# Performance work log

Hardware: AMD Instinct MI355X
Metric: run time of the kernel (lower is better)

## Reference

```python
import jax, jax.numpy as jnp
import numpy as np

C = 512
NUM_GROUPS = 32
EPS = 1e-6


def setup_inputs() -> dict:
    key = jax.random.key(0)
    ks = jax.random.split(key, 6)
    B, H, W = 4, 64, 64
    x = jax.random.normal(ks[0], (B, H, W, C), dtype=jnp.float32)
    # GroupNorm affine params (flax default init: scale=1, bias=0)
    gn_scale = jnp.ones((C,), jnp.float32)
    gn_bias = jnp.zeros((C,), jnp.float32)
    # 1x1 convs == per-pixel dense layers; weight [C_in, C_out], bias [C_out]
    def dense(k):
        return jax.random.normal(k, (C, C), dtype=jnp.float32) * 0.02
    wq, wk, wv, wo = dense(ks[1]), dense(ks[2]), dense(ks[3]), dense(ks[4])
    bq = jnp.zeros((C,), jnp.float32)
    bk = jnp.zeros((C,), jnp.float32)
    bv = jnp.zeros((C,), jnp.float32)
    bo = jnp.zeros((C,), jnp.float32)
    return {"x": x, "gn_scale": gn_scale, "gn_bias": gn_bias,
            "wq": wq, "bq": bq, "wk": wk, "bk": bk,
            "wv": wv, "bv": bv, "wo": wo, "bo": bo}


def _group_norm(x, scale, bias):
    B, H, W, Cc = x.shape
    g = NUM_GROUPS
    xg = x.reshape(B, H, W, g, Cc // g)
    mean = jnp.mean(xg, axis=(1, 2, 4), keepdims=True)
    var = jnp.var(xg, axis=(1, 2, 4), keepdims=True)
    xn = (xg - mean) * jax.lax.rsqrt(var + EPS)
    xn = xn.reshape(B, H, W, Cc)
    return xn * scale + bias


def reference(x, gn_scale, gn_bias, wq, bq, wk, bk, wv, bv, wo, bo):
    B, H, W, Cc = x.shape
    hn = _group_norm(x, gn_scale, gn_bias)
    # 1x1 convs
    q = (hn @ wq + bq).reshape(B, H * W, Cc)
    k = (hn @ wk + bk).reshape(B, H * W, Cc)
    v = (hn @ wv + bv).reshape(B, H * W, Cc)
    scale = jnp.asarray(Cc, x.dtype) ** -0.5
    # scores[b,i,j] = <q_i, k_j> * c^-0.5; softmax over keys j
    attn = jax.nn.softmax(jnp.einsum('bic,bjc->bij', q, k) * scale, axis=-1)
    out = jnp.einsum('bij,bjc->bic', attn, v).reshape(B, H, W, Cc)
    return x + (out @ wo + bo)
```

## Files before the change

kernel.cpp:

```cpp
#include <hip/hip_runtime.h>


typedef __attribute__((ext_vector_type(8))) __bf16 bf16x8;
typedef __attribute__((ext_vector_type(4))) __bf16 bf16x4;
typedef __attribute__((ext_vector_type(4))) float  floatx4;

#define C_DIM 512
#define SPB   4096
#define MTOT  16384

#define HN_OFF  ((size_t)0)
#define Q_OFF   ((size_t)16 << 20)
#define K_OFF   ((size_t)32 << 20)
#define V4_OFF  ((size_t)48 << 20)
#define WT_OFF  ((size_t)64 << 20)
#define O1_OFF  ((size_t)68 << 20)
#define ML_OFF  ((size_t)84 << 20)
#define GS_OFF  (ML_OFF + (size_t)(256 << 10))

__device__ inline floatx4 mfma16(bf16x8 a, bf16x8 b, floatx4 c) {
    return __builtin_amdgcn_mfma_f32_16x16x32_bf16(a, b, c, 0, 0, 0);
}

__device__ inline void gload16(const void* g, void* lds) {
    __builtin_amdgcn_global_load_lds(
        (const __attribute__((address_space(1))) unsigned int*)g,
        (__attribute__((address_space(3))) unsigned int*)lds, 16, 0, 0);
}

__global__ __launch_bounds__(256) void zero_stats(float* gstats) {
    gstats[threadIdx.x] = 0.f;
}

__global__ __launch_bounds__(256) void gn_stats(
    const float* __restrict__ x, float* __restrict__ gstats) {
    int bg = blockIdx.x;
    int b = bg >> 5, g = bg & 31;
    int tid = threadIdx.x;
    int cq = tid & 3, s0 = tid >> 2;
    const float* base = x + (size_t)b * SPB * C_DIM + g * 16 + cq * 4
                          + (size_t)blockIdx.y * 1024 * C_DIM;
    float sum = 0.f, sq = 0.f;
#pragma unroll 4
    for (int i = 0; i < 16; ++i) {
        floatx4 v = *(const floatx4*)(base + (size_t)(i * 64 + s0) * C_DIM);
        sum += v[0] + v[1] + v[2] + v[3];
        sq  += v[0]*v[0] + v[1]*v[1] + v[2]*v[2] + v[3]*v[3];
    }
#pragma unroll
    for (int off = 1; off < 64; off <<= 1) {
        sum += __shfl_xor(sum, off);
        sq  += __shfl_xor(sq,  off);
    }
    __shared__ float sm[8];
    int w = tid >> 6, lane = tid & 63;
    if (lane == 0) { sm[w] = sum; sm[4 + w] = sq; }
    __syncthreads();
    if (tid == 0) {
        atomicAdd(&gstats[bg * 2],     sm[0] + sm[1] + sm[2] + sm[3]);
        atomicAdd(&gstats[bg * 2 + 1], sm[4] + sm[5] + sm[6] + sm[7]);
    }
}

__global__ __launch_bounds__(256) void gn_apply(
    const float* __restrict__ x, const float* __restrict__ gstats,
    const float* __restrict__ gsc, const float* __restrict__ gbi,
    __bf16* __restrict__ hn) {
    int bg = blockIdx.x;
    int b = bg >> 5, g = bg & 31;
    int tid = threadIdx.x;
    int cq = tid & 3, s0 = tid >> 2;
    float S  = gstats[bg * 2], Qs = gstats[bg * 2 + 1];
    float mean = S * (1.f / 65536.f);
    float var  = Qs * (1.f / 65536.f) - mean * mean;
    float rstd = rsqrtf(var + 1e-6f);
    float sc[4], bi[4];
#pragma unroll
    for (int j = 0; j < 4; ++j) {
        float s_ = gsc[g * 16 + cq * 4 + j] * rstd;
        sc[j] = s_;
        bi[j] = gbi[g * 16 + cq * 4 + j] - mean * s_;
    }
    size_t off = (size_t)b * SPB * C_DIM + g * 16 + cq * 4
               + (size_t)blockIdx.y * 1024 * C_DIM;
    const float* base = x + off;
    __bf16* hbase = hn + off;
#pragma unroll 4
    for (int i = 0; i < 16; ++i) {
        floatx4 v = *(const floatx4*)(base + (size_t)(i * 64 + s0) * C_DIM);
        bf16x4 o;
#pragma unroll
        for (int j = 0; j < 4; ++j) o[j] = (__bf16)(v[j] * sc[j] + bi[j]);
        *(bf16x4*)(hbase + (size_t)(i * 64 + s0) * C_DIM) = o;
    }
}

__global__ __launch_bounds__(256) void wt_kernel(
    const float* __restrict__ w0, const float* __restrict__ w1,
    const float* __restrict__ w2, const float* __restrict__ w3,
    __bf16* __restrict__ wt) {
    const float* srcs[4] = {w0, w1, w2, w3};
    const float* src = srcs[blockIdx.z];
    __bf16* dst = wt + (size_t)blockIdx.z * C_DIM * C_DIM;
    __shared__ float tile[32][33];
    int tx = threadIdx.x & 31, ty = threadIdx.x >> 5;
    int gx = blockIdx.x * 32, gy = blockIdx.y * 32;
#pragma unroll
    for (int i = 0; i < 4; ++i)
        tile[ty + i * 8][tx] = src[(size_t)(gy + ty + i * 8) * C_DIM + gx + tx];
    __syncthreads();
#pragma unroll
    for (int i = 0; i < 4; ++i) {
        int n = gx + ty + i * 8;
        int k = gy + tx;
        dst[(size_t)n * C_DIM + k] = (__bf16)tile[tx][ty + i * 8];
    }
}

__global__ __launch_bounds__(256, 2) void proj_qkv(
    const __bf16* __restrict__ hn, const __bf16* __restrict__ wt_all,
    const float* __restrict__ bq, const float* __restrict__ bk,
    const float* __restrict__ bv, __bf16* __restrict__ qout,
    __bf16* __restrict__ kout, __bf16* __restrict__ v4out) {
    int z = blockIdx.z;
    const __bf16* wt = wt_all + (size_t)z * C_DIM * C_DIM;
    const float* bias = (z == 0) ? bq : (z == 1) ? bk : bv;
    __shared__ __bf16 Alds[128 * 32];
    __shared__ __bf16 Blds[128 * 32];
    int tid = threadIdx.x, lane = tid & 63, w = tid >> 6;
    int c = lane & 15, quad = lane >> 4;
    int wm = w & 1, wn = w >> 1;
    int mbase = blockIdx.x * 128, nbase = blockIdx.y * 128;
    floatx4 acc[4][4] = {};
    for (int kb = 0; kb < 16; ++kb) {
        __syncthreads();
#pragma unroll
        for (int p = 0; p < 2; ++p) {
            int chunk0 = w * 128 + p * 64;
            int chunk = chunk0 + lane;
            int row = chunk >> 2, qk = chunk & 3;
            gload16(hn + (size_t)(mbase + row) * C_DIM + kb * 32 + qk * 8, Alds + chunk0 * 8);
            gload16(wt + (size_t)(nbase + row) * C_DIM + kb * 32 + qk * 8, Blds + chunk0 * 8);
        }
        __syncthreads();
        bf16x8 af[4], bfr[4];
#pragma unroll
        for (int mt = 0; mt < 4; ++mt)
            af[mt] = *(const bf16x8*)(Alds + (wm * 64 + mt * 16 + c) * 32 + quad * 8);
#pragma unroll
        for (int nt = 0; nt < 4; ++nt)
            bfr[nt] = *(const bf16x8*)(Blds + (wn * 64 + nt * 16 + c) * 32 + quad * 8);
#pragma unroll
        for (int mt = 0; mt < 4; ++mt)
#pragma unroll
            for (int nt = 0; nt < 4; ++nt)
                acc[mt][nt] = mfma16(af[mt], bfr[nt], acc[mt][nt]);
    }
    float scale = (z == 0) ? 0.0441941738241592f : 1.0f;
#pragma unroll
    for (int nt = 0; nt < 4; ++nt) {
        int n = nbase + wn * 64 + nt * 16 + c;
        float bval = bias[n];
#pragma unroll
        for (int mt = 0; mt < 4; ++mt) {
            int m0 = mbase + wm * 64 + mt * 16 + quad * 4;
#pragma unroll
            for (int r = 0; r < 4; ++r) {
                int m = m0 + r;
                float val = (acc[mt][nt][r] + bval) * scale;
                if (z == 0)      qout[(size_t)m * C_DIM + n] = (__bf16)val;
                else if (z == 1) kout[(size_t)m * C_DIM + n] = (__bf16)val;
                else {
                    int bb = m >> 12, pos = m & 4095;
                    v4out[((size_t)(bb * 512 + (pos >> 3)) * C_DIM + n) * 8 + (pos & 7)] = (__bf16)val;
                }
            }
        }
    }
}

__device__ inline void stage_K(const __bf16* kbase, int key0,
                               __bf16* Klds, int w, int lane) {
#pragma unroll
    for (int p = 0; p < 8; ++p) {
        int chunk0 = w * 512 + p * 64;
        int chunk = chunk0 + lane;
        gload16(kbase + (size_t)(key0 + (chunk & 31)) * C_DIM + (chunk >> 5) * 8,
                Klds + chunk0 * 8);
    }
}

__device__ inline void stage_V(const __bf16* vsrc, __bf16* Vlds, int w, int lane) {
#pragma unroll
    for (int p = 0; p < 8; ++p) {
        int chunk0 = w * 512 + p * 64;
        gload16(vsrc + (size_t)(chunk0 + lane) * 8, Vlds + chunk0 * 8);
    }
}

__global__ __launch_bounds__(256, 2) void flash_kernel(
    const __bf16* __restrict__ q, const __bf16* __restrict__ kmat,
    const __bf16* __restrict__ v4, __bf16* __restrict__ op0,
    __bf16* __restrict__ op1, float* __restrict__ lpart) {
    __shared__ __bf16 Klds[16384];
    __shared__ __bf16 Vlds[16384];
    __shared__ __bf16 Plds[64 * 40];
    int tid = threadIdx.x, lane = tid & 63, w = tid >> 6;
    int c = lane & 15, quad = lane >> 4;
    int bid = blockIdx.x;
    int h = bid & 1, qt = (bid >> 1) & 63, b = bid >> 7;

    const __bf16* qp = q + ((size_t)(b * SPB + qt * 64 + w * 16 + c)) * C_DIM + quad * 8;
    bf16x8 qf[16];
#pragma unroll
    for (int ks = 0; ks < 16; ++ks) qf[ks] = *(const bf16x8*)(qp + ks * 32);
    floatx4 o[4][8];
#pragma unroll
    for (int mg = 0; mg < 4; ++mg)
#pragma unroll
        for (int t = 0; t < 8; ++t) o[mg][t] = (floatx4){0.f, 0.f, 0.f, 0.f};
    float l_r[4] = {0.f, 0.f, 0.f, 0.f};

    const __bf16* kbase = kmat + (size_t)b * SPB * C_DIM;
    const __bf16* vbase = v4 + (size_t)b * 512 * C_DIM * 8;

    stage_K(kbase, h * 2048, Klds, w, lane);
    __syncthreads();

    for (int kt = 0; kt < 64; ++kt) {
        int key0 = h * 2048 + kt * 32;
        stage_V(vbase + (size_t)(key0 >> 3) * C_DIM * 8, Vlds, w, lane);
        floatx4 s0 = (floatx4){0.f,0.f,0.f,0.f}, s1 = (floatx4){0.f,0.f,0.f,0.f};
#pragma unroll
        for (int ks = 0; ks < 16; ++ks) {
            bf16x8 k0 = *(const bf16x8*)(Klds + (((ks * 4 + quad) * 32) + c) * 8);
            bf16x8 k1 = *(const bf16x8*)(Klds + (((ks * 4 + quad) * 32) + c + 16) * 8);
            s0 = mfma16(qf[ks], k0, s0);
            s1 = mfma16(qf[ks], k1, s1);
        }
#pragma unroll
        for (int r = 0; r < 4; ++r) {
            float p0 = __expf(s0[r]);
            float p1 = __expf(s1[r]);
            l_r[r] += p0 + p1;
            int row = w * 16 + quad * 4 + r;
            Plds[row * 40 + c]      = (__bf16)p0;
            Plds[row * 40 + c + 16] = (__bf16)p1;
        }
        __syncthreads();
        int kn = (kt < 63) ? kt + 1 : 63;
        stage_K(kbase, h * 2048 + kn * 32, Klds, w, lane);
        bf16x8 pf[4];
#pragma unroll
        for (int mg = 0; mg < 4; ++mg)
            pf[mg] = *(const bf16x8*)(Plds + (mg * 16 + c) * 40 + quad * 8);
#pragma unroll
        for (int t = 0; t < 8; ++t) {
            bf16x8 vf = *(const bf16x8*)(Vlds + ((size_t)quad * 512 + w * 128 + t * 16 + c) * 8);
#pragma unroll
            for (int mg = 0; mg < 4; ++mg)
                o[mg][t] = mfma16(pf[mg], vf, o[mg][t]);
        }
        __syncthreads();
    }
#pragma unroll
    for (int r = 0; r < 4; ++r) {
        float l = l_r[r];
        l += __shfl_xor(l, 1);
        l += __shfl_xor(l, 2);
        l += __shfl_xor(l, 4);
        l += __shfl_xor(l, 8);
        l_r[r] = l;
    }
    if (c == 0) {
#pragma unroll
        for (int r = 0; r < 4; ++r) {
            int grow = b * SPB + qt * 64 + w * 16 + quad * 4 + r;
            lpart[h * MTOT + grow] = l_r[r];
        }
    }
    __bf16* ob = h ? op1 : op0;
#pragma unroll
    for (int mg = 0; mg < 4; ++mg)
#pragma unroll
        for (int t = 0; t < 8; ++t)
#pragma unroll
            for (int r = 0; r < 4; ++r) {
                int grow = b * SPB + qt * 64 + mg * 16 + quad * 4 + r;
                ob[(size_t)grow * C_DIM + w * 128 + t * 16 + c] = (__bf16)o[mg][t][r];
            }
}

__global__ __launch_bounds__(256) void combine_kernel(
    const __bf16* __restrict__ o0, const __bf16* __restrict__ o1,
    const float* __restrict__ lpart, __bf16* __restrict__ attn) {
    int tid = threadIdx.x, lane = tid & 63, w = tid >> 6;
    int rbase = blockIdx.x * 64 + w * 16;
    for (int rr = 0; rr < 16; ++rr) {
        int row = rbase + rr;
        float inv = 1.f / (lpart[row] + lpart[MTOT + row]);
        bf16x8 v0 = *(const bf16x8*)(o0 + (size_t)row * C_DIM + lane * 8);
        bf16x8 v1 = *(const bf16x8*)(o1 + (size_t)row * C_DIM + lane * 8);
        bf16x8 r;
#pragma unroll
        for (int j = 0; j < 8; ++j) r[j] = (__bf16)(((float)v0[j] + (float)v1[j]) * inv);
        *(bf16x8*)(attn + (size_t)row * C_DIM + lane * 8) = r;
    }
}

__global__ __launch_bounds__(256, 2) void proj_out(
    const __bf16* __restrict__ attn, const __bf16* __restrict__ wot,
    const float* __restrict__ bo, const float* __restrict__ x,
    float* __restrict__ out) {
    __shared__ __bf16 Alds[128 * 32];
    __shared__ __bf16 Blds[128 * 32];
    int tid = threadIdx.x, lane = tid & 63, w = tid >> 6;
    int c = lane & 15, quad = lane >> 4;
    int wm = w & 1, wn = w >> 1;
    int mbase = blockIdx.x * 128, nbase = blockIdx.y * 128;
    floatx4 acc[4][4] = {};
    for (int kb = 0; kb < 16; ++kb) {
        __syncthreads();
#pragma unroll
        for (int p = 0; p < 2; ++p) {
            int chunk0 = w * 128 + p * 64;
            int chunk = chunk0 + lane;
            int row = chunk >> 2, qk = chunk & 3;
            gload16(attn + (size_t)(mbase + row) * C_DIM + kb * 32 + qk * 8, Alds + chunk0 * 8);
            gload16(wot + (size_t)(nbase + row) * C_DIM + kb * 32 + qk * 8, Blds + chunk0 * 8);
        }
        __syncthreads();
        bf16x8 af[4], bfr[4];
#pragma unroll
        for (int mt = 0; mt < 4; ++mt)
            af[mt] = *(const bf16x8*)(Alds + (wm * 64 + mt * 16 + c) * 32 + quad * 8);
#pragma unroll
        for (int nt = 0; nt < 4; ++nt)
            bfr[nt] = *(const bf16x8*)(Blds + (wn * 64 + nt * 16 + c) * 32 + quad * 8);
#pragma unroll
        for (int mt = 0; mt < 4; ++mt)
#pragma unroll
            for (int nt = 0; nt < 4; ++nt)
                acc[mt][nt] = mfma16(af[mt], bfr[nt], acc[mt][nt]);
    }
#pragma unroll
    for (int nt = 0; nt < 4; ++nt) {
        int n = nbase + wn * 64 + nt * 16 + c;
        float bval = bo[n];
#pragma unroll
        for (int mt = 0; mt < 4; ++mt) {
            int m0 = mbase + wm * 64 + mt * 16 + quad * 4;
#pragma unroll
            for (int r = 0; r < 4; ++r) {
                size_t idx = (size_t)(m0 + r) * C_DIM + n;
                out[idx] = acc[mt][nt][r] + bval + x[idx];
            }
        }
    }
}

extern "C" void kernel_launch(void* const* d_in, const int* in_sizes, int n_in,
                              void* d_out, int out_size, void* d_ws, size_t ws_size,
                              hipStream_t stream) {
    const float* x   = (const float*)d_in[0];
    const float* gsc = (const float*)d_in[1];
    const float* gbi = (const float*)d_in[2];
    const float* wq  = (const float*)d_in[3];
    const float* bq  = (const float*)d_in[4];
    const float* wk  = (const float*)d_in[5];
    const float* bk  = (const float*)d_in[6];
    const float* wv  = (const float*)d_in[7];
    const float* bv  = (const float*)d_in[8];
    const float* wo  = (const float*)d_in[9];
    const float* bo  = (const float*)d_in[10];
    char* ws = (char*)d_ws;
    __bf16* hn  = (__bf16*)(ws + HN_OFF);
    __bf16* qb  = (__bf16*)(ws + Q_OFF);
    __bf16* kb  = (__bf16*)(ws + K_OFF);
    __bf16* v4  = (__bf16*)(ws + V4_OFF);
    __bf16* wt  = (__bf16*)(ws + WT_OFF);
    __bf16* op0 = (__bf16*)(ws + HN_OFF);
    __bf16* op1 = (__bf16*)(ws + O1_OFF);
    float*  lp  = (float*)(ws + ML_OFF);
    float*  gs  = (float*)(ws + GS_OFF);
    __bf16* attn = qb;
    float* out = (float*)d_out;

    zero_stats<<<1, 256, 0, stream>>>(gs);
    wt_kernel<<<dim3(16, 16, 4), 256, 0, stream>>>(wq, wk, wv, wo, wt);
    gn_stats<<<dim3(128, 4), 256, 0, stream>>>(x, gs);
    gn_apply<<<dim3(128, 4), 256, 0, stream>>>(x, gs, gsc, gbi, hn);
    proj_qkv<<<dim3(128, 4, 3), 256, 0, stream>>>(hn, wt, bq, bk, bv, qb, kb, v4);
    flash_kernel<<<512, 256, 0, stream>>>(qb, kb, v4, op0, op1, lp);
    combine_kernel<<<256, 256, 0, stream>>>(op0, op1, lp, attn);
    proj_out<<<dim3(128, 4), 256, 0, stream>>>(attn, wt + (size_t)3 * C_DIM * C_DIM, bo, x, out);
}
```

Baseline: 439.2 us.

## Double-buffer K in flash loop, load V to registers, fuse combine into proj_out

The flash kernel now double-buffers K and P tiles in LDS and prefetches V straight into registers, one iteration ahead, instead of staging it through LDS. This drops one barrier per iteration and lets loads overlap the MFMA work. The separate combine kernel is removed: proj_out reads both partial outputs, normalises them by the summed row sums and writes the result into LDS itself. gn_stats also writes a bf16 copy of x that gn_apply reads instead of the fp32 input, halving gn_apply's reads at the cost of extra writes in gn_stats; the register-held V buffers raise register pressure.

```diff
diff --git a/kernel.cpp b/kernel.cpp
--- a/kernel.cpp
+++ b/kernel.cpp
@@ -33,24 +33,31 @@
 }
 
 __global__ __launch_bounds__(256) void gn_stats(
-    const float* __restrict__ x, float* __restrict__ gstats) {
+    const float* __restrict__ x, float* __restrict__ gstats,
+    __bf16* __restrict__ xb) {
     int bg = blockIdx.x;
     int b = bg >> 5, g = bg & 31;
     int tid = threadIdx.x;
     int cq = tid & 3, s0 = tid >> 2;
-    const float* base = x + (size_t)b * SPB * C_DIM + g * 16 + cq * 4
-                          + (size_t)blockIdx.y * 1024 * C_DIM;
+    size_t off = (size_t)b * SPB * C_DIM + g * 16 + cq * 4
+               + (size_t)blockIdx.y * 1024 * C_DIM;
+    const float* base = x + off;
+    __bf16* xbb = xb + off;
     float sum = 0.f, sq = 0.f;
 #pragma unroll 4
     for (int i = 0; i < 16; ++i) {
         floatx4 v = *(const floatx4*)(base + (size_t)(i * 64 + s0) * C_DIM);
         sum += v[0] + v[1] + v[2] + v[3];
         sq  += v[0]*v[0] + v[1]*v[1] + v[2]*v[2] + v[3]*v[3];
-    }
-#pragma unroll
-    for (int off = 1; off < 64; off <<= 1) {
-        sum += __shfl_xor(sum, off);
-        sq  += __shfl_xor(sq,  off);
+        bf16x4 o;
+#pragma unroll
+        for (int j = 0; j < 4; ++j) o[j] = (__bf16)v[j];
+        *(bf16x4*)(xbb + (size_t)(i * 64 + s0) * C_DIM) = o;
+    }
+#pragma unroll
+    for (int off2 = 1; off2 < 64; off2 <<= 1) {
+        sum += __shfl_xor(sum, off2);
+        sq  += __shfl_xor(sq,  off2);
     }
     __shared__ float sm[8];
     int w = tid >> 6, lane = tid & 63;
@@ -63,7 +70,7 @@
 }
 
 __global__ __launch_bounds__(256) void gn_apply(
-    const float* __restrict__ x, const float* __restrict__ gstats,
+    const __bf16* __restrict__ xb, const float* __restrict__ gstats,
     const float* __restrict__ gsc, const float* __restrict__ gbi,
     __bf16* __restrict__ hn) {
     int bg = blockIdx.x;
@@ -83,14 +90,14 @@
     }
     size_t off = (size_t)b * SPB * C_DIM + g * 16 + cq * 4
                + (size_t)blockIdx.y * 1024 * C_DIM;
-    const float* base = x + off;
+    const __bf16* base = xb + off;
     __bf16* hbase = hn + off;
 #pragma unroll 4
     for (int i = 0; i < 16; ++i) {
-        floatx4 v = *(const floatx4*)(base + (size_t)(i * 64 + s0) * C_DIM);
+        bf16x4 v = *(const bf16x4*)(base + (size_t)(i * 64 + s0) * C_DIM);
         bf16x4 o;
 #pragma unroll
-        for (int j = 0; j < 4; ++j) o[j] = (__bf16)(v[j] * sc[j] + bi[j]);
+        for (int j = 0; j < 4; ++j) o[j] = (__bf16)((float)v[j] * sc[j] + bi[j]);
         *(bf16x4*)(hbase + (size_t)(i * 64 + s0) * C_DIM) = o;
     }
 }
@@ -180,21 +187,13 @@
 }
 
 __device__ inline void stage_K(const __bf16* kbase, int key0,
-                               __bf16* Klds, int w, int lane) {
+                               __bf16* Kl, int w, int lane) {
 #pragma unroll
     for (int p = 0; p < 8; ++p) {
         int chunk0 = w * 512 + p * 64;
         int chunk = chunk0 + lane;
         gload16(kbase + (size_t)(key0 + (chunk & 31)) * C_DIM + (chunk >> 5) * 8,
-                Klds + chunk0 * 8);
-    }
-}
-
-__device__ inline void stage_V(const __bf16* vsrc, __bf16* Vlds, int w, int lane) {
-#pragma unroll
-    for (int p = 0; p < 8; ++p) {
-        int chunk0 = w * 512 + p * 64;
-        gload16(vsrc + (size_t)(chunk0 + lane) * 8, Vlds + chunk0 * 8);
+                Kl + chunk0 * 8);
     }
 }
 
@@ -202,13 +201,14 @@
     const __bf16* __restrict__ q, const __bf16* __restrict__ kmat,
     const __bf16* __restrict__ v4, __bf16* __restrict__ op0,
     __bf16* __restrict__ op1, float* __restrict__ lpart) {
-    __shared__ __bf16 Klds[16384];
-    __shared__ __bf16 Vlds[16384];
-    __shared__ __bf16 Plds[64 * 40];
+    __shared__ __bf16 Klds[2][16384];
+    __shared__ __bf16 Plds[2][64 * 40];
     int tid = threadIdx.x, lane = tid & 63, w = tid >> 6;
     int c = lane & 15, quad = lane >> 4;
     int bid = blockIdx.x;
     int h = bid & 1, qt = (bid >> 1) & 63, b = bid >> 7;
+    int hk = h * 2048;
+    int wch = w * 128;
 
     const __bf16* qp = q + ((size_t)(b * SPB + qt * 64 + w * 16 + c)) * C_DIM + quad * 8;
     bf16x8 qf[16];
@@ -224,45 +224,58 @@
     const __bf16* kbase = kmat + (size_t)b * SPB * C_DIM;
     const __bf16* vbase = v4 + (size_t)b * 512 * C_DIM * 8;
 
-    stage_K(kbase, h * 2048, Klds, w, lane);
+    bf16x8 vA[8], vB[8];
+    stage_K(kbase, hk, &Klds[0][0], w, lane);
+    stage_K(kbase, hk + 32, &Klds[1][0], w, lane);
+#pragma unroll
+    for (int t = 0; t < 8; ++t)
+        vA[t] = *(const bf16x8*)(vbase + ((size_t)((hk >> 3) + quad) * 512 + wch + t * 16 + c) * 8);
     __syncthreads();
 
-    for (int kt = 0; kt < 64; ++kt) {
-        int key0 = h * 2048 + kt * 32;
-        stage_V(vbase + (size_t)(key0 >> 3) * C_DIM * 8, Vlds, w, lane);
+    auto iter = [&](int kt, int KB, bf16x8* vuse, bf16x8* vnext) {
+        const __bf16* KL = &Klds[KB][0];
         floatx4 s0 = (floatx4){0.f,0.f,0.f,0.f}, s1 = (floatx4){0.f,0.f,0.f,0.f};
 #pragma unroll
         for (int ks = 0; ks < 16; ++ks) {
-            bf16x8 k0 = *(const bf16x8*)(Klds + (((ks * 4 + quad) * 32) + c) * 8);
-            bf16x8 k1 = *(const bf16x8*)(Klds + (((ks * 4 + quad) * 32) + c + 16) * 8);
+            bf16x8 k0 = *(const bf16x8*)(KL + (((ks * 4 + quad) * 32) + c) * 8);
+            bf16x8 k1 = *(const bf16x8*)(KL + (((ks * 4 + quad) * 32) + c + 16) * 8);
             s0 = mfma16(qf[ks], k0, s0);
             s1 = mfma16(qf[ks], k1, s1);
         }
+        __bf16* PL = &Plds[KB][0];
 #pragma unroll
         for (int r = 0; r < 4; ++r) {
             float p0 = __expf(s0[r]);
             float p1 = __expf(s1[r]);
             l_r[r] += p0 + p1;
             int row = w * 16 + quad * 4 + r;
-            Plds[row * 40 + c]      = (__bf16)p0;
-            Plds[row * 40 + c + 16] = (__bf16)p1;
+            PL[row * 40 + c]      = (__bf16)p0;
+            PL[row * 40 + c + 16] = (__bf16)p1;
         }
         __syncthreads();
-        int kn = (kt < 63) ? kt + 1 : 63;
-        stage_K(kbase, h * 2048 + kn * 32, Klds, w, lane);
+        int kf = (kt + 2 < 64) ? kt + 2 : 63;
+        stage_K(kbase, hk + kf * 32, &Klds[KB][0], w, lane);
+        int kv = (kt + 1 < 64) ? kt + 1 : 63;
+        int vk0 = hk + kv * 32;
+#pragma unroll
+        for (int t = 0; t < 8; ++t)
+            vnext[t] = *(const bf16x8*)(vbase + ((size_t)((vk0 >> 3) + quad) * 512 + wch + t * 16 + c) * 8);
         bf16x8 pf[4];
 #pragma unroll
         for (int mg = 0; mg < 4; ++mg)
-            pf[mg] = *(const bf16x8*)(Plds + (mg * 16 + c) * 40 + quad * 8);
-#pragma unroll
-        for (int t = 0; t < 8; ++t) {
-            bf16x8 vf = *(const bf16x8*)(Vlds + ((size_t)quad * 512 + w * 128 + t * 16 + c) * 8);
+            pf[mg] = *(const bf16x8*)(PL + (mg * 16 + c) * 40 + quad * 8);
+#pragma unroll
+        for (int t = 0; t < 8; ++t)
 #pragma unroll
             for (int mg = 0; mg < 4; ++mg)
-                o[mg][t] = mfma16(pf[mg], vf, o[mg][t]);
-        }
-        __syncthreads();
-    }
+                o[mg][t] = mfma16(pf[mg], vuse[t], o[mg][t]);
+    };
+
+    for (int kt2 = 0; kt2 < 32; ++kt2) {
+        iter(2 * kt2,     0, vA, vB);
+        iter(2 * kt2 + 1, 1, vB, vA);
+    }
+
 #pragma unroll
     for (int r = 0; r < 4; ++r) {
         float l = l_r[r];
@@ -287,46 +300,48 @@
 #pragma unroll
             for (int r = 0; r < 4; ++r) {
                 int grow = b * SPB + qt * 64 + mg * 16 + quad * 4 + r;
-                ob[(size_t)grow * C_DIM + w * 128 + t * 16 + c] = (__bf16)o[mg][t][r];
+                ob[(size_t)grow * C_DIM + wch + t * 16 + c] = (__bf16)o[mg][t][r];
             }
 }
 
-__global__ __launch_bounds__(256) void combine_kernel(
+__global__ __launch_bounds__(256, 2) void proj_out(
     const __bf16* __restrict__ o0, const __bf16* __restrict__ o1,
-    const float* __restrict__ lpart, __bf16* __restrict__ attn) {
-    int tid = threadIdx.x, lane = tid & 63, w = tid >> 6;
-    int rbase = blockIdx.x * 64 + w * 16;
-    for (int rr = 0; rr < 16; ++rr) {
-        int row = rbase + rr;
-        float inv = 1.f / (lpart[row] + lpart[MTOT + row]);
-        bf16x8 v0 = *(const bf16x8*)(o0 + (size_t)row * C_DIM + lane * 8);
-        bf16x8 v1 = *(const bf16x8*)(o1 + (size_t)row * C_DIM + lane * 8);
-        bf16x8 r;
-#pragma unroll
-        for (int j = 0; j < 8; ++j) r[j] = (__bf16)(((float)v0[j] + (float)v1[j]) * inv);
-        *(bf16x8*)(attn + (size_t)row * C_DIM + lane * 8) = r;
-    }
-}
-
-__global__ __launch_bounds__(256, 2) void proj_out(
-    const __bf16* __restrict__ attn, const __bf16* __restrict__ wot,
+    const float* __restrict__ lp, const __bf16* __restrict__ wot,
     const float* __restrict__ bo, const float* __restrict__ x,
     float* __restrict__ out) {
     __shared__ __bf16 Alds[128 * 32];
     __shared__ __bf16 Blds[128 * 32];
+    __shared__ float linv[128];
     int tid = threadIdx.x, lane = tid & 63, w = tid >> 6;
     int c = lane & 15, quad = lane >> 4;
     int wm = w & 1, wn = w >> 1;
     int mbase = blockIdx.x * 128, nbase = blockIdx.y * 128;
+    if (tid < 128) {
+        int row = mbase + tid;
+        linv[tid] = 1.f / (lp[row] + lp[MTOT + row]);
+    }
     floatx4 acc[4][4] = {};
     for (int kb = 0; kb < 16; ++kb) {
         __syncthreads();
+#pragma unroll
+        for (int p = 0; p < 2; ++p) {
+            int chunk = tid + p * 256;
+            int row = chunk >> 2, qk = chunk & 3;
+            size_t gidx = (size_t)(mbase + row) * C_DIM + kb * 32 + qk * 8;
+            bf16x8 a0 = *(const bf16x8*)(o0 + gidx);
+            bf16x8 a1 = *(const bf16x8*)(o1 + gidx);
+            float s = linv[row];
+            bf16x8 rr;
+#pragma unroll
+            for (int j = 0; j < 8; ++j)
+                rr[j] = (__bf16)(((float)a0[j] + (float)a1[j]) * s);
+            *(bf16x8*)(Alds + chunk * 8) = rr;
+        }
 #pragma unroll
         for (int p = 0; p < 2; ++p) {
             int chunk0 = w * 128 + p * 64;
             int chunk = chunk0 + lane;
             int row = chunk >> 2, qk = chunk & 3;
-            gload16(attn + (size_t)(mbase + row) * C_DIM + kb * 32 + qk * 8, Alds + chunk0 * 8);
             gload16(wot + (size_t)(nbase + row) * C_DIM + kb * 32 + qk * 8, Blds + chunk0 * 8);
         }
         __syncthreads();
@@ -381,17 +396,17 @@
     __bf16* wt  = (__bf16*)(ws + WT_OFF);
     __bf16* op0 = (__bf16*)(ws + HN_OFF);
     __bf16* op1 = (__bf16*)(ws + O1_OFF);
+    __bf16* xb  = (__bf16*)(ws + O1_OFF);
     float*  lp  = (float*)(ws + ML_OFF);
     float*  gs  = (float*)(ws + GS_OFF);
-    __bf16* attn = qb;
     float* out = (float*)d_out;
 
     zero_stats<<<1, 256, 0, stream>>>(gs);
     wt_kernel<<<dim3(16, 16, 4), 256, 0, stream>>>(wq, wk, wv, wo, wt);
-    gn_stats<<<dim3(128, 4), 256, 0, stream>>>(x, gs);
-    gn_apply<<<dim3(128, 4), 256, 0, stream>>>(x, gs, gsc, gbi, hn);
+    gn_stats<<<dim3(128, 4), 256, 0, stream>>>(x, gs, xb);
+    gn_apply<<<dim3(128, 4), 256, 0, stream>>>(xb, gs, gsc, gbi, hn);
     proj_qkv<<<dim3(128, 4, 3), 256, 0, stream>>>(hn, wt, bq, bk, bv, qb, kb, v4);
     flash_kernel<<<512, 256, 0, stream>>>(qb, kb, v4, op0, op1, lp);
-    combine_kernel<<<256, 256, 0, stream>>>(op0, op1, lp, attn);
-    proj_out<<<dim3(128, 4), 256, 0, stream>>>(attn, wt + (size_t)3 * C_DIM * C_DIM, bo, x, out);
-}
+    proj_out<<<dim3(128, 4), 256, 0, stream>>>(op0, op1, lp,
+        wt + (size_t)3 * C_DIM * C_DIM, bo, x, out);
+}
```

Result: slower. 943.6 us (+114.9%).
